# Kernel tuning notes

Hardware: AMD Instinct MI355X
Metric: run time of the kernel (lower is better)

The kernel has to match this reference:

```python
import jax, jax.numpy as jnp
import numpy as np

ABOVE_MAX_DOY_VALUE = 10000
MTF_FOR_HPF = 0.4
MAX_MASKED_RATE = 0.5
UP_FACTOR = 2


def _psf_kernel(c: int, mtf_fc: float) -> jnp.ndarray:
    """Gaussian PSF kernel whose MTF at Nyquist (fc = 0.5/mtf_res) equals mtf_fc.
    mtf_res = res = 1.0 -> half_kernel_width = 1 -> 3x3 kernel, identical per channel."""
    mtf_res = 1.0
    # sigma = sqrt(-ln(mtf_fc)) / (sqrt(2) * pi * fc), fc = 0.5 / mtf_res
    sigma = mtf_res * np.sqrt(-2.0 * np.log(mtf_fc)) / np.pi
    hkw = int(np.ceil(mtf_res / 1.0))  # = 1
    coords = np.arange(-hkw, hkw + 1, dtype=np.float64)
    d2 = coords[:, None] ** 2 + coords[None, :] ** 2
    k = np.exp(-d2 / (2.0 * sigma * sigma))
    k = (k / k.sum()).astype(np.float32)
    return jnp.asarray(np.broadcast_to(k, (c, 1) + k.shape).copy())  # [c,1,3,3]


def setup_inputs() -> dict:
    key = jax.random.key(0)
    k1, k2, k3, k4 = jax.random.split(key, 4)
    lr_data = jax.random.normal(k1, (1, 20, 4, 256, 256), dtype=jnp.float32)
    hr_data = jax.random.normal(k2, (1, 30, 4, 512, 512), dtype=jnp.float32)
    # unique, sorted DOYs; every lr date has >=2 strictly earlier hr dates
    lr_doy = (30 + 16 * jnp.arange(20, dtype=jnp.int32))[None, :]   # 30..334
    hr_doy = (1 + 12 * jnp.arange(30, dtype=jnp.int32))[None, :]    # 1..349
    lr_mask = jax.random.uniform(k3, (1, 20, 256, 256)) < 0.05
    hr_mask = jax.random.uniform(k4, (1, 30, 512, 512)) < 0.08  # rate < 0.5 everywhere
    return {"lr_data": lr_data, "hr_data": hr_data, "lr_doy": lr_doy,
            "hr_doy": hr_doy, "lr_mask": lr_mask, "hr_mask": hr_mask}


def reference(lr_data, hr_data, lr_doy, hr_doy, lr_mask, hr_mask):
    b, t_lr, c, h0, w0 = lr_data.shape
    H, W = h0 * UP_FACTOR, w0 * UP_FACTOR
    t_hr = hr_data.shape[1]

    # DateWiseSITSModule: bilinear upsampling of data, nearest for mask
    lr_up = jax.image.resize(lr_data, (b, t_lr, c, H, W), method="linear")
    lr_mask_up = jax.image.resize(lr_mask.astype(jnp.float32), (b, t_lr, H, W),
                                  method="nearest") > 0.5

    # DOY difference matrix [t_hr, t_lr]; negative (hr after lr) -> ABOVE
    diff = lr_doy[0, None, :] - hr_doy[0, :, None]
    diff = jnp.where(diff < 0, ABOVE_MAX_DOY_VALUE, diff)
    # exclude heavily masked hr frames
    rate = hr_mask.astype(jnp.float32).mean(axis=(-1, -2))[0]  # [t_hr]
    diff = jnp.where((rate > MAX_MASKED_RATE)[:, None], ABOVE_MAX_DOY_VALUE, diff)

    first_min = diff.min(axis=0)
    first_idx = diff.argmin(axis=0)                         # [t_lr]
    first_vals = hr_doy[0, first_idx]                       # [t_lr]
    # mask out the first minimum (vectorized form of the per-column loop)
    diff2 = diff.at[first_idx, jnp.arange(t_lr)].set(ABOVE_MAX_DOY_VALUE)
    second_min = diff2.min(axis=0)
    second_idx = diff2.argmin(axis=0)
    second_vals = hr_doy[0, second_idx]

    valid = (first_min < ABOVE_MAX_DOY_VALUE) & (second_min < ABOVE_MAX_DOY_VALUE)

    masked_first = hr_mask[:, first_idx]                    # [b,t_lr,H,W]
    masked_second = hr_mask[:, second_idx]

    g1 = hr_data[:, first_idx]                              # [b,t_lr,c,H,W]
    g2 = hr_data[:, second_idx]
    fv = first_vals.astype(lr_data.dtype)[None, :, None, None, None]
    sv = second_vals.astype(lr_data.dtype)[None, :, None, None, None]
    coef_a = (g2 - g1) / (sv - fv)
    coef_b = g2 - coef_a * sv
    doy_f = lr_doy.astype(lr_data.dtype)[:, :, None, None, None]
    predicted_hr = coef_a * doy_f + coef_b                  # [b,t_lr,c,H,W]

    # high-pass filter: x - depthwise PSF lowpass
    kernel = _psf_kernel(c, MTF_FOR_HPF)                    # [c,1,3,3]
    x = predicted_hr.reshape(b * t_lr, c, H, W)
    low = jax.lax.conv_general_dilated(x, kernel, (1, 1), "SAME",
                                       feature_group_count=c)
    hpf = (x - low).reshape(b, t_lr, c, H, W)

    final_mask = (lr_mask_up
                  | (~valid)[None, :, None, None]
                  | masked_first
                  | masked_second)
    final_hr = lr_up + hpf
    return final_hr, final_mask, lr_up
```

## Files before the change

### kernel.cpp

```cpp
#include <hip/hip_runtime.h>
#include <math.h>

#define T_LR 20
#define T_HR 30
#define CCH  4
#define H0   256
#define W0   256
#define HH   512
#define WW   512
#define ABOVE 10000

typedef float f32x4 __attribute__((ext_vector_type(4)));

#define WS_FIDX  0
#define WS_SIDX  32
#define WS_ALPHA 64
#define WS_BETA  96
#define WS_VALID 128
#define WS_CNT   160

__global__ void rate_kernel(const int* __restrict__ hr_mask,
                            int* __restrict__ wsi) {
    int j = blockIdx.x >> 3;
    int slice = blockIdx.x & 7;
    const int elems = HH * WW / 8;
    const uint4* p = (const uint4*)(hr_mask + (size_t)j * HH * WW + (size_t)slice * elems);
    int sum = 0;
    for (int e = threadIdx.x; e < elems / 4; e += blockDim.x) {
        uint4 v = p[e];
        sum += (int)(v.x + v.y + v.z + v.w);
    }
    for (int o = 32; o; o >>= 1) sum += __shfl_down(sum, o);
    __shared__ int ssum[4];
    if ((threadIdx.x & 63) == 0) ssum[threadIdx.x >> 6] = sum;
    __syncthreads();
    if (threadIdx.x == 0)
        wsi[WS_CNT + blockIdx.x] = ssum[0] + ssum[1] + ssum[2] + ssum[3];
}

__global__ void select_kernel(const int* __restrict__ lr_doy,
                              const int* __restrict__ hr_doy,
                              float* __restrict__ ws) {
    int i = threadIdx.x;
    if (i >= T_LR) return;
    const int* wsi_c = (const int*)ws;
    int doy = lr_doy[i];

    int fmin = ABOVE, fidx = 0;
    for (int j = 0; j < T_HR; j++) {
        int d = doy - hr_doy[j];
        if (d < 0) d = ABOVE;
        int cnt = 0;
        for (int k = 0; k < 8; k++) cnt += wsi_c[WS_CNT + 8 * j + k];
        float rate = (float)cnt / (float)(HH * WW);
        if (rate > 0.5f) d = ABOVE;
        if (d < fmin) { fmin = d; fidx = j; }
    }
    int smin = ABOVE, sidx = 0;
    for (int j = 0; j < T_HR; j++) {
        int d = doy - hr_doy[j];
        if (d < 0) d = ABOVE;
        int cnt = 0;
        for (int k = 0; k < 8; k++) cnt += wsi_c[WS_CNT + 8 * j + k];
        float rate = (float)cnt / (float)(HH * WW);
        if (rate > 0.5f) d = ABOVE;
        if (j == fidx) d = ABOVE;
        if (d < smin) { smin = d; sidx = j; }
    }
    int valid = (fmin < ABOVE) && (smin < ABOVE);
    float fv = (float)hr_doy[fidx], sv = (float)hr_doy[sidx];
    float denom = sv - fv;

    int* wsi = (int*)ws;
    wsi[WS_FIDX + i] = fidx;
    wsi[WS_SIDX + i] = sidx;
    ws[WS_ALPHA + i] = (sv - (float)doy) / denom;
    ws[WS_BETA + i]  = ((float)doy - fv) / denom;
    wsi[WS_VALID + i] = valid;
}

__launch_bounds__(256)
__global__ void fuse_kernel(const float* __restrict__ lr_data,
                            const float* __restrict__ hr_data,
                            const int* __restrict__ lr_mask,
                            const int* __restrict__ hr_mask,
                            const float* __restrict__ ws,
                            float* __restrict__ out,
                            float wc, float we, float wk) {
    const int lin = blockIdx.x + (blockIdx.y << 4) + (blockIdx.z << 8);
    const int q = lin >> 3;
    const int z = (lin & 7) * 10 + (q >> 8);
    const int t = q & 255;
    const int i  = z >> 2;
    const int ch = z & 3;
    const int x0 = (t & 15) * 32;
    const int y0 = (t >> 4) * 32;
    const int tid = threadIdx.x;

    const int* wsi = (const int*)ws;
    const int f       = wsi[WS_FIDX + i];
    const int s       = wsi[WS_SIDX + i];
    const float alpha = ws[WS_ALPHA + i];
    const float beta  = ws[WS_BETA + i];
    const int valid   = wsi[WS_VALID + i];

    __shared__ float sh[2][34][44];
    __shared__ float shl[18][28];

    const float* g0 = hr_data + ((size_t)f * CCH + ch) * HH * WW;
    const float* g1 = hr_data + ((size_t)s * CCH + ch) * HH * WW;

    for (int e = tid; e < 2 * 340; e += 256) {
        int img = e >= 340;
        int e2 = e - img * 340;
        int r = e2 / 10, c4 = e2 - r * 10;
        int gy = y0 - 1 + r;
        int gx0 = x0 - 4 + c4 * 4;
        float4 v = make_float4(0.f, 0.f, 0.f, 0.f);
        if (gy >= 0 && gy < HH && gx0 >= 0 && gx0 < WW)
            v = *(const float4*)((img ? g1 : g0) + (size_t)gy * WW + gx0);
        *(float4*)&sh[img][r][c4 * 4] = v;
    }

    const int ly0 = (y0 >> 1) - 1, lx0c = (x0 >> 1) - 4;
    const float* lp = lr_data + ((size_t)i * CCH + ch) * H0 * W0;
    if (tid < 18 * 6) {
        int r = tid / 6, c4 = tid - r * 6;
        int gy = min(max(ly0 + r, 0), H0 - 1);
        int gx0 = lx0c + c4 * 4;
        float4 v;
        if (gx0 >= 0 && gx0 + 3 < W0) {
            v = *(const float4*)(lp + (size_t)gy * W0 + gx0);
        } else {
            v.x = lp[(size_t)gy * W0 + min(max(gx0 + 0, 0), W0 - 1)];
            v.y = lp[(size_t)gy * W0 + min(max(gx0 + 1, 0), W0 - 1)];
            v.z = lp[(size_t)gy * W0 + min(max(gx0 + 2, 0), W0 - 1)];
            v.w = lp[(size_t)gy * W0 + min(max(gx0 + 3, 0), W0 - 1)];
        }
        *(float4*)&shl[r][c4 * 4] = v;
    }
    __syncthreads();

    const int ty = tid >> 3, tx4 = tid & 7;
    const int y = y0 + ty, x = x0 + tx4 * 4;
    const int c = tx4 * 4 + 4;

    float hp[2][4];
    #pragma unroll
    for (int img = 0; img < 2; img++) {
        float win[3][6];
        #pragma unroll
        for (int rr = 0; rr < 3; rr++) {
            const float* row = sh[img][ty + rr];
            float4 v  = *(const float4*)&row[c];
            float2 a2 = *(const float2*)&row[c - 2];
            float2 b2 = *(const float2*)&row[c + 4];
            win[rr][0] = a2.y;
            win[rr][1] = v.x; win[rr][2] = v.y; win[rr][3] = v.z; win[rr][4] = v.w;
            win[rr][5] = b2.x;
        }
        #pragma unroll
        for (int k = 0; k < 4; k++) {
            float center = win[1][k + 1];
            float low =
                wk * (win[0][k] + win[0][k + 2] + win[2][k] + win[2][k + 2]) +
                we * (win[0][k + 1] + win[2][k + 1] + win[1][k] + win[1][k + 2]) +
                wc * center;
            hp[img][k] = center - low;
        }
    }

    const int jy = y >> 1;
    const int lr_c = jy - ly0;
    const int lr_n = jy + ((y & 1) ? 1 : -1) - ly0;
    const int c0 = tx4 * 2 + 4;

    float ma = 0.75f * shl[lr_c][c0 - 1] + 0.25f * shl[lr_n][c0 - 1];
    float mb = 0.75f * shl[lr_c][c0    ] + 0.25f * shl[lr_n][c0    ];
    float mc = 0.75f * shl[lr_c][c0 + 1] + 0.25f * shl[lr_n][c0 + 1];
    float md = 0.75f * shl[lr_c][c0 + 2] + 0.25f * shl[lr_n][c0 + 2];

    f32x4 lu;
    lu.x = 0.75f * mb + 0.25f * ma;
    lu.y = 0.75f * mb + 0.25f * mc;
    lu.z = 0.75f * mc + 0.25f * mb;
    lu.w = 0.75f * mc + 0.25f * md;

    const size_t outM  = (size_t)T_LR * CCH * HH * WW;
    const size_t outLU = outM + (size_t)T_LR * HH * WW;
    const size_t oidx = (((size_t)i * CCH + ch) * HH + y) * WW + x;

    f32x4 fh;
    fh.x = lu.x + alpha * hp[0][0] + beta * hp[1][0];
    fh.y = lu.y + alpha * hp[0][1] + beta * hp[1][1];
    fh.z = lu.z + alpha * hp[0][2] + beta * hp[1][2];
    fh.w = lu.w + alpha * hp[0][3] + beta * hp[1][3];
    __builtin_nontemporal_store(fh, (f32x4*)&out[oidx]);
    __builtin_nontemporal_store(lu, (f32x4*)&out[outLU + oidx]);

    if (ch == 0) {
        int4 mf = *(const int4*)(hr_mask + ((size_t)f * HH + y) * WW + x);
        int4 ms = *(const int4*)(hr_mask + ((size_t)s * HH + y) * WW + x);
        const int* lm = lr_mask + ((size_t)i * H0 + jy) * W0;
        int gjx0 = x >> 1;
        int m0 = lm[gjx0], m1 = lm[gjx0 + 1];
        int nv = !valid;
        f32x4 mo;
        mo.x = (m0 | mf.x | ms.x | nv) ? 1.f : 0.f;
        mo.y = (m0 | mf.y | ms.y | nv) ? 1.f : 0.f;
        mo.z = (m1 | mf.z | ms.z | nv) ? 1.f : 0.f;
        mo.w = (m1 | mf.w | ms.w | nv) ? 1.f : 0.f;
        __builtin_nontemporal_store(mo, (f32x4*)&out[outM + ((size_t)i * HH + y) * WW + x]);
    }
}

extern "C" void kernel_launch(void* const* d_in, const int* in_sizes, int n_in,
                              void* d_out, int out_size, void* d_ws, size_t ws_size,
                              hipStream_t stream) {
    const float* lr_data = (const float*)d_in[0];
    const float* hr_data = (const float*)d_in[1];
    const int* lr_doy    = (const int*)d_in[2];
    const int* hr_doy    = (const int*)d_in[3];
    const int* lr_mask   = (const int*)d_in[4];
    const int* hr_mask   = (const int*)d_in[5];
    float* out = (float*)d_out;
    float* ws  = (float*)d_ws;
    int* wsi   = (int*)d_ws;

    double sigma = sqrt(-2.0 * log(0.4)) / M_PI;
    double e1 = exp(-1.0 / (2.0 * sigma * sigma));
    double e2 = exp(-2.0 / (2.0 * sigma * sigma));
    double ssum = 1.0 + 4.0 * e1 + 4.0 * e2;
    float wc = (float)(1.0 / ssum);
    float we = (float)(e1 / ssum);
    float wk = (float)(e2 / ssum);

    rate_kernel<<<T_HR * 8, 256, 0, stream>>>(hr_mask, wsi);
    select_kernel<<<1, 64, 0, stream>>>(lr_doy, hr_doy, ws);

    dim3 grid(WW / 32, HH / 32, T_LR * CCH);
    fuse_kernel<<<grid, 256, 0, stream>>>(lr_data, hr_data, lr_mask, hr_mask,
                                          ws, out, wc, we, wk);
}
```

Baseline: 88.02 us.

## Separate Gaussian PSF into horizontal then vertical passes and pre-interpolate LR rows

The 3x3 Gaussian low-pass is factored into a horizontal 1D pass, applied while loading the HR tile into shared memory, and a vertical 1D pass applied from shared memory. The lr bilinear upsampling does its horizontal interpolation during the staging step, so the per-thread work drops to a vertical blend. Together these cut arithmetic and shared-memory traffic per output. The costs are an extra global load of the HR centre pixels, scalar halo loads at the tile edges, and slight floating-point differences from the separable form.

```diff
diff --git a/kernel.cpp b/kernel.cpp
--- a/kernel.cpp
+++ b/kernel.cpp
@@ -86,7 +86,7 @@
                             const int* __restrict__ hr_mask,
                             const float* __restrict__ ws,
                             float* __restrict__ out,
-                            float wc, float we, float wk) {
+                            float ga, float gb) {
     const int lin = blockIdx.x + (blockIdx.y << 4) + (blockIdx.z << 8);
     const int q = lin >> 3;
     const int z = (lin & 7) * 10 + (q >> 8);
@@ -104,97 +104,78 @@
     const float beta  = ws[WS_BETA + i];
     const int valid   = wsi[WS_VALID + i];
 
-    __shared__ float sh[2][34][44];
-    __shared__ float shl[18][28];
+    __shared__ float Hs[2][34][36];
+    __shared__ float hxs[18][36];
 
     const float* g0 = hr_data + ((size_t)f * CCH + ch) * HH * WW;
     const float* g1 = hr_data + ((size_t)s * CCH + ch) * HH * WW;
 
-    for (int e = tid; e < 2 * 340; e += 256) {
-        int img = e >= 340;
-        int e2 = e - img * 340;
-        int r = e2 / 10, c4 = e2 - r * 10;
-        int gy = y0 - 1 + r;
-        int gx0 = x0 - 4 + c4 * 4;
-        float4 v = make_float4(0.f, 0.f, 0.f, 0.f);
-        if (gy >= 0 && gy < HH && gx0 >= 0 && gx0 < WW)
-            v = *(const float4*)((img ? g1 : g0) + (size_t)gy * WW + gx0);
-        *(float4*)&sh[img][r][c4 * 4] = v;
-    }
-
-    const int ly0 = (y0 >> 1) - 1, lx0c = (x0 >> 1) - 4;
-    const float* lp = lr_data + ((size_t)i * CCH + ch) * H0 * W0;
-    if (tid < 18 * 6) {
-        int r = tid / 6, c4 = tid - r * 6;
+    for (int e = tid; e < 544; e += 256) {
+        int img = e >= 272;
+        int e2 = e - img * 272;
+        int rr = e2 >> 3, tq = e2 & 7;
+        int gy = y0 - 1 + rr;
+        f32x4 H = {0.f, 0.f, 0.f, 0.f};
+        if (gy >= 0 && gy < HH) {
+            const float* gp = (img ? g1 : g0) + (size_t)gy * WW;
+            int gx = x0 + tq * 4;
+            f32x4 v = *(const f32x4*)(gp + gx);
+            float xl = (gx > 0)       ? gp[gx - 1] : 0.f;
+            float xr = (gx + 4 < WW)  ? gp[gx + 4] : 0.f;
+            H.x = ga * (xl  + v.y) + gb * v.x;
+            H.y = ga * (v.x + v.z) + gb * v.y;
+            H.z = ga * (v.y + v.w) + gb * v.z;
+            H.w = ga * (v.z + xr ) + gb * v.w;
+        }
+        *(f32x4*)&Hs[img][rr][tq * 4] = H;
+    }
+
+    const int ly0 = (y0 >> 1) - 1;
+    if (tid < 144) {
+        int r = tid >> 3, tq = tid & 7;
         int gy = min(max(ly0 + r, 0), H0 - 1);
-        int gx0 = lx0c + c4 * 4;
-        float4 v;
-        if (gx0 >= 0 && gx0 + 3 < W0) {
-            v = *(const float4*)(lp + (size_t)gy * W0 + gx0);
-        } else {
-            v.x = lp[(size_t)gy * W0 + min(max(gx0 + 0, 0), W0 - 1)];
-            v.y = lp[(size_t)gy * W0 + min(max(gx0 + 1, 0), W0 - 1)];
-            v.z = lp[(size_t)gy * W0 + min(max(gx0 + 2, 0), W0 - 1)];
-            v.w = lp[(size_t)gy * W0 + min(max(gx0 + 3, 0), W0 - 1)];
-        }
-        *(float4*)&shl[r][c4 * 4] = v;
+        const float* lp = lr_data + ((size_t)i * CCH + ch) * H0 * W0 + (size_t)gy * W0;
+        int J = (x0 >> 1) + tq * 2;
+        float vm = lp[max(J - 1, 0)];
+        float v0 = lp[J];
+        float v1 = lp[J + 1];
+        float v2 = lp[min(J + 2, W0 - 1)];
+        f32x4 hx;
+        hx.x = 0.75f * v0 + 0.25f * vm;
+        hx.y = 0.75f * v0 + 0.25f * v1;
+        hx.z = 0.75f * v1 + 0.25f * v0;
+        hx.w = 0.75f * v1 + 0.25f * v2;
+        *(f32x4*)&hxs[r][tq * 4] = hx;
     }
     __syncthreads();
 
     const int ty = tid >> 3, tx4 = tid & 7;
     const int y = y0 + ty, x = x0 + tx4 * 4;
-    const int c = tx4 * 4 + 4;
-
-    float hp[2][4];
-    #pragma unroll
-    for (int img = 0; img < 2; img++) {
-        float win[3][6];
-        #pragma unroll
-        for (int rr = 0; rr < 3; rr++) {
-            const float* row = sh[img][ty + rr];
-            float4 v  = *(const float4*)&row[c];
-            float2 a2 = *(const float2*)&row[c - 2];
-            float2 b2 = *(const float2*)&row[c + 4];
-            win[rr][0] = a2.y;
-            win[rr][1] = v.x; win[rr][2] = v.y; win[rr][3] = v.z; win[rr][4] = v.w;
-            win[rr][5] = b2.x;
-        }
-        #pragma unroll
-        for (int k = 0; k < 4; k++) {
-            float center = win[1][k + 1];
-            float low =
-                wk * (win[0][k] + win[0][k + 2] + win[2][k] + win[2][k + 2]) +
-                we * (win[0][k + 1] + win[2][k + 1] + win[1][k] + win[1][k + 2]) +
-                wc * center;
-            hp[img][k] = center - low;
-        }
-    }
+    const int c = tx4 * 4;
+
+    f32x4 hu0 = *(const f32x4*)&Hs[0][ty    ][c];
+    f32x4 hm0 = *(const f32x4*)&Hs[0][ty + 1][c];
+    f32x4 hd0 = *(const f32x4*)&Hs[0][ty + 2][c];
+    f32x4 hu1 = *(const f32x4*)&Hs[1][ty    ][c];
+    f32x4 hm1 = *(const f32x4*)&Hs[1][ty + 1][c];
+    f32x4 hd1 = *(const f32x4*)&Hs[1][ty + 2][c];
+    f32x4 xc0 = *(const f32x4*)(g0 + (size_t)y * WW + x);
+    f32x4 xc1 = *(const f32x4*)(g1 + (size_t)y * WW + x);
+    f32x4 hp0 = xc0 - (ga * (hu0 + hd0) + gb * hm0);
+    f32x4 hp1 = xc1 - (ga * (hu1 + hd1) + gb * hm1);
 
     const int jy = y >> 1;
-    const int lr_c = jy - ly0;
-    const int lr_n = jy + ((y & 1) ? 1 : -1) - ly0;
-    const int c0 = tx4 * 2 + 4;
-
-    float ma = 0.75f * shl[lr_c][c0 - 1] + 0.25f * shl[lr_n][c0 - 1];
-    float mb = 0.75f * shl[lr_c][c0    ] + 0.25f * shl[lr_n][c0    ];
-    float mc = 0.75f * shl[lr_c][c0 + 1] + 0.25f * shl[lr_n][c0 + 1];
-    float md = 0.75f * shl[lr_c][c0 + 2] + 0.25f * shl[lr_n][c0 + 2];
-
-    f32x4 lu;
-    lu.x = 0.75f * mb + 0.25f * ma;
-    lu.y = 0.75f * mb + 0.25f * mc;
-    lu.z = 0.75f * mc + 0.25f * mb;
-    lu.w = 0.75f * mc + 0.25f * md;
+    const int rc = jy - ly0;
+    const int rn = jy + ((y & 1) ? 1 : -1) - ly0;
+    f32x4 ha = *(const f32x4*)&hxs[rc][c];
+    f32x4 hb = *(const f32x4*)&hxs[rn][c];
+    f32x4 lu = 0.75f * ha + 0.25f * hb;
 
     const size_t outM  = (size_t)T_LR * CCH * HH * WW;
     const size_t outLU = outM + (size_t)T_LR * HH * WW;
     const size_t oidx = (((size_t)i * CCH + ch) * HH + y) * WW + x;
 
-    f32x4 fh;
-    fh.x = lu.x + alpha * hp[0][0] + beta * hp[1][0];
-    fh.y = lu.y + alpha * hp[0][1] + beta * hp[1][1];
-    fh.z = lu.z + alpha * hp[0][2] + beta * hp[1][2];
-    fh.w = lu.w + alpha * hp[0][3] + beta * hp[1][3];
+    f32x4 fh = lu + alpha * hp0 + beta * hp1;
     __builtin_nontemporal_store(fh, (f32x4*)&out[oidx]);
     __builtin_nontemporal_store(lu, (f32x4*)&out[outLU + oidx]);
 
@@ -229,16 +210,14 @@
 
     double sigma = sqrt(-2.0 * log(0.4)) / M_PI;
     double e1 = exp(-1.0 / (2.0 * sigma * sigma));
-    double e2 = exp(-2.0 / (2.0 * sigma * sigma));
-    double ssum = 1.0 + 4.0 * e1 + 4.0 * e2;
-    float wc = (float)(1.0 / ssum);
-    float we = (float)(e1 / ssum);
-    float wk = (float)(e2 / ssum);
+    double axis_sum = 1.0 + 2.0 * e1;
+    float ga = (float)(e1 / axis_sum);
+    float gb = (float)(1.0 / axis_sum);
 
     rate_kernel<<<T_HR * 8, 256, 0, stream>>>(hr_mask, wsi);
     select_kernel<<<1, 64, 0, stream>>>(lr_doy, hr_doy, ws);
 
     dim3 grid(WW / 32, HH / 32, T_LR * CCH);
     fuse_kernel<<<grid, 256, 0, stream>>>(lr_data, hr_data, lr_mask, hr_mask,
-                                          ws, out, wc, we, wk);
-}
+                                          ws, out, ga, gb);
+}
```

New measurement: 80.02 us. 1.1x faster.
